# Optimization experiments

Hardware: AMD Instinct MI355X
Metric: run time of the kernel (lower is better)

## Reference

```python
import jax, jax.numpy as jnp
import numpy as np

N, IN, OUT, K = 4096, 512, 256, 3
ALPHA, BETA, ETA = 0.2, 0.1, 0.5
NEG_INF = -9e15


def setup_inputs() -> dict:
    key = jax.random.key(0)
    k1, k2, k3, k4, k5, k6 = jax.random.split(key, 6)
    h = jax.random.normal(k1, (N, IN), dtype=jnp.float32)
    # xavier-ish scale for params
    W = jax.random.normal(k2, (K * IN, OUT), dtype=jnp.float32) * (1.414 / np.sqrt(IN + OUT))
    a = jax.random.normal(k3, (2 * OUT * K, 1), dtype=jnp.float32) * 0.05
    disc = jax.random.normal(k4, (2 * OUT, 1), dtype=jnp.float32) * 0.05
    k_mask = jax.random.randint(k5, (K, N, N), 0, 2).astype(jnp.int32)  # 0/1 k-hop masks
    lamda = jax.random.uniform(k6, (1,), dtype=jnp.float32)
    return {"h": h, "W": W, "a": a, "disc": disc, "k_mask": k_mask, "lamda": lamda}


def reference(h, W, a, disc, k_mask, lamda):
    lam = lamda[0]
    Wk = W.reshape(K, IN, OUT)          # W[i*IN:(i+1)*IN] per hop
    ak = a.reshape(K, 2, OUT)           # a[2*hop*OUT:(2*hop+2)*OUT] per hop, split in two
    d = disc.reshape(2, OUT)

    # Per-hop projections. In the torch loop Wh is recomputed from h each hop,
    # so only hop 0 determines the returned features; all hops feed dischange.
    Wh_all = jnp.einsum('ni,kio->kno', h, Wk)  # [K, N, OUT]

    # dischange = sum_i eta^i * (Wh_i @ d1 + (Wh_i @ d2).T)  -- rank-1 separable
    wts = ETA ** jnp.arange(K, dtype=jnp.float32)            # [K]
    dv1 = jnp.einsum('kno,o->kn', Wh_all, d[0])              # [K, N]
    dv2 = jnp.einsum('kno,o->kn', Wh_all, d[1])
    u = jnp.einsum('k,kn->n', wts, dv1)
    v = jnp.einsum('k,kn->n', wts, dv2)
    dischange = u[:, None] + v[None, :]                      # [N, N]

    # hop-0 masked GAT attention
    Wh0 = Wh_all[0]
    s1 = Wh0 @ ak[0, 0]                                      # [N]
    s2 = Wh0 @ ak[0, 1]
    e = jax.nn.leaky_relu(s1[:, None] + s2[None, :], ALPHA)  # [N, N]
    att = jax.nn.softmax(jnp.where(k_mask[0] > 0, e, NEG_INF), axis=1)
    # dropout disabled (eval mode / training=False)
    Wh = (1.0 - BETA) * (att @ Wh0) + BETA * Wh0
    out = jax.nn.elu(Wh)

    # normalize dischange and threshold against lamda
    dn = dischange / jnp.maximum(jnp.abs(dischange.min()), dischange.max())
    pos = (dn > lam).astype(jnp.int32)
    dn = jnp.where(dn > lam, 0.0, dn)
    neg = (dn < -lam).astype(jnp.int32)
    dn = jnp.where(dn < -lam, 0.0, dn)

    # mask lists computed from ORIGINAL masks, then applied sequentially
    pos_list = [((k_mask[i] + pos) >= 2).astype(jnp.int32) for i in range(K - 1)]
    neg_list = [((k_mask[i] + neg) >= 2).astype(jnp.int32) for i in range(1, K)]
    km = k_mask
    for i in range(1, K):
        km = km.at[i].add(pos_list[i - 1])
        km = km.at[i - 1].add(-pos_list[i - 1])
    for i in range(K - 1):
        km = km.at[i + 1].add(neg_list[i])
        km = km.at[i].add(-neg_list[i])

    return out, dn, km
```

## Files before the change

### kernel.cpp

```cpp
#include <hip/hip_runtime.h>
#include <hip/hip_bf16.h>
#include <math.h>

#define N 4096
#define DIN 512
#define DOUT 256

typedef short bf16x8 __attribute__((ext_vector_type(8)));
typedef float f32x4 __attribute__((ext_vector_type(4)));

static __device__ __forceinline__ unsigned short f2bf(float x) {
  __hip_bfloat16 b = __float2bfloat16(x);
  return __builtin_bit_cast(unsigned short, b);
}

__global__ __launch_bounds__(256) void k_pq(const float* __restrict__ W,
                                            const float* __restrict__ disc,
                                            double* __restrict__ p, double* __restrict__ q) {
  __shared__ double lds[8];
  int i = blockIdx.x;
  int t = threadIdx.x;
  double accp = 0.0, accq = 0.0;
  const double wts[3] = {1.0, 0.5, 0.25};
#pragma unroll
  for (int k = 0; k < 3; ++k) {
    double w = (double)W[((size_t)(k * DIN + i)) * DOUT + t];
    accp += wts[k] * w * (double)disc[t];
    accq += wts[k] * w * (double)disc[DOUT + t];
  }
  for (int off = 32; off; off >>= 1) { accp += __shfl_down(accp, off); accq += __shfl_down(accq, off); }
  int l = t & 63, w_ = t >> 6;
  if (l == 0) { lds[w_] = accp; lds[4 + w_] = accq; }
  __syncthreads();
  if (t == 0) {
    p[i] = lds[0] + lds[1] + lds[2] + lds[3];
    q[i] = lds[4] + lds[5] + lds[6] + lds[7];
  }
}

__global__ __launch_bounds__(256) void k_uv(const float* __restrict__ h,
                                            const double* __restrict__ p, const double* __restrict__ q,
                                            double* __restrict__ u, double* __restrict__ v) {
  __shared__ double lds[8];
  int n = blockIdx.x, t = threadIdx.x;
  double su = 0.0, sv = 0.0;
#pragma unroll
  for (int i = t; i < DIN; i += 256) {
    double hv = (double)h[(size_t)n * DIN + i];
    su += hv * p[i];
    sv += hv * q[i];
  }
  for (int off = 32; off; off >>= 1) { su += __shfl_down(su, off); sv += __shfl_down(sv, off); }
  int l = t & 63, w_ = t >> 6;
  if (l == 0) { lds[w_] = su; lds[4 + w_] = sv; }
  __syncthreads();
  if (t == 0) {
    u[n] = lds[0] + lds[1] + lds[2] + lds[3];
    v[n] = lds[4] + lds[5] + lds[6] + lds[7];
  }
}

__global__ __launch_bounds__(1024) void k_denom(const double* __restrict__ u,
                                                const double* __restrict__ v,
                                                double* __restrict__ scal) {
  __shared__ double lds[64];
  int t = threadIdx.x;
  double mnu = 1e300, mxu = -1e300, mnv = 1e300, mxv = -1e300;
#pragma unroll
  for (int k = 0; k < 4; ++k) {
    double uu = u[t + k * 1024], vv = v[t + k * 1024];
    mnu = fmin(mnu, uu); mxu = fmax(mxu, uu);
    mnv = fmin(mnv, vv); mxv = fmax(mxv, vv);
  }
  for (int off = 32; off; off >>= 1) {
    mnu = fmin(mnu, __shfl_down(mnu, off)); mxu = fmax(mxu, __shfl_down(mxu, off));
    mnv = fmin(mnv, __shfl_down(mnv, off)); mxv = fmax(mxv, __shfl_down(mxv, off));
  }
  int l = t & 63, w_ = t >> 6;
  if (l == 0) { lds[w_] = mnu; lds[16 + w_] = mxu; lds[32 + w_] = mnv; lds[48 + w_] = mxv; }
  __syncthreads();
  if (t == 0) {
    double a = 1e300, b = -1e300, c = 1e300, d = -1e300;
    for (int k = 0; k < 16; ++k) {
      a = fmin(a, lds[k]); b = fmax(b, lds[16 + k]);
      c = fmin(c, lds[32 + k]); d = fmax(d, lds[48 + k]);
    }
    double mn = a + c, mx = b + d;
    double denom = fmax(fabs(mn), mx);
    scal[0] = 1.0 / denom;
  }
}

__global__ __launch_bounds__(256) void k_dnkm(const int* __restrict__ kmask,
                                              const double* __restrict__ u, const double* __restrict__ v,
                                              const double* __restrict__ scal, const float* __restrict__ lamda,
                                              float* __restrict__ dn, float* __restrict__ kmout) {
  const size_t NN = (size_t)N * N;
  const int* k0 = kmask; const int* k1 = kmask + NN; const int* k2 = kmask + 2 * NN;
  float* km0 = kmout; float* km1 = kmout + NN; float* km2 = kmout + 2 * NN;
  const size_t total4 = NN / 4;
  double inv = scal[0];
  double lam = (double)lamda[0];
  for (size_t idx = (size_t)blockIdx.x * 256 + threadIdx.x; idx < total4;
       idx += (size_t)gridDim.x * 256) {
    int i = (int)(idx >> 10);
    int j = (int)(idx & 1023) << 2;
    size_t base = (size_t)i * N + j;
    double ui = u[i];
    double2 va = *(const double2*)(v + j);
    double2 vb = *(const double2*)(v + j + 2);
    double vv[4] = {va.x, va.y, vb.x, vb.y};
    int4 m0 = *(const int4*)(k0 + base);
    int4 m1 = *(const int4*)(k1 + base);
    int4 m2 = *(const int4*)(k2 + base);
    float4 odn, o0, o1, o2;
#pragma unroll
    for (int c = 0; c < 4; ++c) {
      double dnv = (ui + vv[c]) * inv;
      bool pos = dnv > lam, neg = dnv < -lam;
      float dnf = (pos || neg) ? 0.0f : (float)dnv;
      int mk0 = (&m0.x)[c], mk1 = (&m1.x)[c], mk2 = (&m2.x)[c];
      int p0 = pos ? mk0 : 0;
      int p1 = pos ? mk1 : 0;
      int n0 = neg ? mk1 : 0;
      int n1 = neg ? mk2 : 0;
      (&odn.x)[c] = dnf;
      (&o0.x)[c] = (float)(mk0 - p0 - n0);
      (&o1.x)[c] = (float)(mk1 + p0 - p1 + n0 - n1);
      (&o2.x)[c] = (float)(mk2 + p1 + n1);
    }
    *(float4*)(dn + base) = odn;
    *(float4*)(km0 + base) = o0;
    *(float4*)(km1 + base) = o1;
    *(float4*)(km2 + base) = o2;
  }
}

__global__ __launch_bounds__(256) void k_wh0(const float* __restrict__ h, const float* __restrict__ W,
                                             float* __restrict__ Wh0, unsigned short* __restrict__ Wh0T) {
  __shared__ float As[64][20];
  __shared__ float Bs[16][72];
  int t = threadIdx.x;
  int i0 = blockIdx.x * 64, o0 = blockIdx.y * 64;
  int tx = t & 15, ty = t >> 4;
  float acc[4][4] = {};
  int am = t >> 2, ak = (t & 3) * 4;
  int bk = t >> 4, bn = (t & 15) * 4;
  for (int kb = 0; kb < DIN; kb += 16) {
    float4 av = *(const float4*)(h + (size_t)(i0 + am) * DIN + kb + ak);
    float4 bv = *(const float4*)(W + (size_t)(kb + bk) * DOUT + o0 + bn);
    *(float4*)&As[am][ak] = av;
    *(float4*)&Bs[bk][bn] = bv;
    __syncthreads();
#pragma unroll
    for (int kk = 0; kk < 16; ++kk) {
      float a0 = As[ty * 4 + 0][kk], a1 = As[ty * 4 + 1][kk];
      float a2 = As[ty * 4 + 2][kk], a3 = As[ty * 4 + 3][kk];
      float4 b = *(const float4*)&Bs[kk][tx * 4];
      acc[0][0] += a0 * b.x; acc[0][1] += a0 * b.y; acc[0][2] += a0 * b.z; acc[0][3] += a0 * b.w;
      acc[1][0] += a1 * b.x; acc[1][1] += a1 * b.y; acc[1][2] += a1 * b.z; acc[1][3] += a1 * b.w;
      acc[2][0] += a2 * b.x; acc[2][1] += a2 * b.y; acc[2][2] += a2 * b.z; acc[2][3] += a2 * b.w;
      acc[3][0] += a3 * b.x; acc[3][1] += a3 * b.y; acc[3][2] += a3 * b.z; acc[3][3] += a3 * b.w;
    }
    __syncthreads();
  }
#pragma unroll
  for (int r = 0; r < 4; ++r) {
    int n = i0 + ty * 4 + r;
    float4 vo = {acc[r][0], acc[r][1], acc[r][2], acc[r][3]};
    *(float4*)(Wh0 + (size_t)n * DOUT + o0 + tx * 4) = vo;
#pragma unroll
    for (int c = 0; c < 4; ++c) {
      Wh0T[(size_t)(o0 + tx * 4 + c) * N + n] = f2bf(acc[r][c]);
    }
  }
}

__global__ __launch_bounds__(256) void k_s1s2(const float* __restrict__ Wh0, const float* __restrict__ a,
                                              float* __restrict__ s1, float* __restrict__ s2) {
  __shared__ float lds[8];
  int i = blockIdx.x, t = threadIdx.x;
  float val = Wh0[(size_t)i * DOUT + t];
  float v1 = val * a[t];
  float v2 = val * a[DOUT + t];
  for (int off = 32; off; off >>= 1) { v1 += __shfl_down(v1, off); v2 += __shfl_down(v2, off); }
  int l = t & 63, w_ = t >> 6;
  if (l == 0) { lds[w_] = v1; lds[4 + w_] = v2; }
  __syncthreads();
  if (t == 0) {
    s1[i] = lds[0] + lds[1] + lds[2] + lds[3];
    s2[i] = lds[4] + lds[5] + lds[6] + lds[7];
  }
}

__global__ __launch_bounds__(256) void k_rowstats(const int* __restrict__ k0,
                                                  const float* __restrict__ s1, const float* __restrict__ s2,
                                                  float* __restrict__ mrow, float* __restrict__ zinv,
                                                  int* __restrict__ flag) {
  __shared__ float earr[N];
  __shared__ float redf[4];
  __shared__ int redi[4];
  __shared__ float bm; __shared__ int bc;
  int i = blockIdx.x, t = threadIdx.x;
  float s1i = s1[i];
  float lmax = -1e30f; int lcnt = 0;
  for (int j = t; j < N; j += 256) {
    int mk = k0[(size_t)i * N + j];
    float sv = s1i + s2[j];
    float e = sv >= 0.0f ? sv : 0.2f * sv;
    bool um = mk > 0;
    earr[j] = um ? e : -1e30f;
    if (um) { lmax = fmaxf(lmax, e); lcnt++; }
  }
  for (int off = 32; off; off >>= 1) { lmax = fmaxf(lmax, __shfl_down(lmax, off)); lcnt += __shfl_down(lcnt, off); }
  int l = t & 63, w_ = t >> 6;
  if (l == 0) { redf[w_] = lmax; redi[w_] = lcnt; }
  __syncthreads();
  if (t == 0) {
    bm = fmaxf(fmaxf(redf[0], redf[1]), fmaxf(redf[2], redf[3]));
    bc = redi[0] + redi[1] + redi[2] + redi[3];
  }
  __syncthreads();
  float m = bm; int c = bc;
  float lsum = 0.0f;
  if (c > 0) {
    for (int j = t; j < N; j += 256) {
      float e = earr[j];
      if (e > -1e29f) lsum += expf(e - m);
    }
  }
  for (int off = 32; off; off >>= 1) lsum += __shfl_down(lsum, off);
  if (l == 0) redf[w_] = lsum;
  __syncthreads();
  if (t == 0) {
    float Z = redf[0] + redf[1] + redf[2] + redf[3];
    if (c == 0) { mrow[i] = 0.0f; zinv[i] = 1.0f / (float)N; flag[i] = 1; }
    else        { mrow[i] = m;    zinv[i] = 1.0f / Z;        flag[i] = 0; }
  }
}

__global__ __launch_bounds__(256) void k_attn(const int* __restrict__ k0,
                                              const float* __restrict__ s1, const float* __restrict__ s2,
                                              const float* __restrict__ mrow, const float* __restrict__ zinv,
                                              const int* __restrict__ flag,
                                              const float* __restrict__ Wh0, const unsigned short* __restrict__ Wh0T,
                                              float* __restrict__ out) {
  __shared__ unsigned short Ats[16][40];
  int t = threadIdx.x;
  int i0 = blockIdx.x * 16;
  int l = t & 63, w = t >> 6;
  int o0 = w * 64;
  int r = t & 15, c2 = t >> 4;
  int irow = i0 + r;
  float s1r = s1[irow], mr = mrow[irow];
  int fl = flag[irow];
  const int* mptr = k0 + (size_t)irow * N + c2 * 2;
  f32x4 acc[4] = {f32x4{0,0,0,0}, f32x4{0,0,0,0}, f32x4{0,0,0,0}, f32x4{0,0,0,0}};
  const unsigned short* bbase = Wh0T + ((size_t)(o0 + (l & 15)) * N + 8 * (l >> 4));
  bf16x8 bn0 = *(const bf16x8*)(bbase + 0 * 16 * N);
  bf16x8 bn1 = *(const bf16x8*)(bbase + 1 * 16 * N);
  bf16x8 bn2 = *(const bf16x8*)(bbase + 2 * 16 * N);
  bf16x8 bn3 = *(const bf16x8*)(bbase + 3 * 16 * N);
  for (int j0 = 0; j0 < N; j0 += 32) {
    int2 mk = *(const int2*)(mptr + j0);
    int j = j0 + c2 * 2;
    float e0 = s1r + s2[j];     e0 = e0 >= 0.0f ? e0 : 0.2f * e0;
    float e1 = s1r + s2[j + 1]; e1 = e1 >= 0.0f ? e1 : 0.2f * e1;
    float p0 = fl ? 1.0f : (mk.x > 0 ? expf(e0 - mr) : 0.0f);
    float p1 = fl ? 1.0f : (mk.y > 0 ? expf(e1 - mr) : 0.0f);
    unsigned int packed = (unsigned int)f2bf(p0) | ((unsigned int)f2bf(p1) << 16);
    *(unsigned int*)(&Ats[r][c2 * 2]) = packed;
    bf16x8 bc0 = bn0, bc1 = bn1, bc2 = bn2, bc3 = bn3;
    if (j0 + 32 < N) {
      const unsigned short* nb = bbase + (j0 + 32);
      bn0 = *(const bf16x8*)(nb + 0 * 16 * N);
      bn1 = *(const bf16x8*)(nb + 1 * 16 * N);
      bn2 = *(const bf16x8*)(nb + 2 * 16 * N);
      bn3 = *(const bf16x8*)(nb + 3 * 16 * N);
    }
    __syncthreads();
    bf16x8 af = *(const bf16x8*)(&Ats[l & 15][8 * (l >> 4)]);
    acc[0] = __builtin_amdgcn_mfma_f32_16x16x32_bf16(af, bc0, acc[0], 0, 0, 0);
    acc[1] = __builtin_amdgcn_mfma_f32_16x16x32_bf16(af, bc1, acc[1], 0, 0, 0);
    acc[2] = __builtin_amdgcn_mfma_f32_16x16x32_bf16(af, bc2, acc[2], 0, 0, 0);
    acc[3] = __builtin_amdgcn_mfma_f32_16x16x32_bf16(af, bc3, acc[3], 0, 0, 0);
    __syncthreads();
  }
  int col = l & 15, rw = (l >> 4) * 4;
#pragma unroll
  for (int reg = 0; reg < 4; ++reg) {
    int i = i0 + rw + reg;
    float zi = zinv[i];
#pragma unroll
    for (int os = 0; os < 4; ++os) {
      int o = o0 + os * 16 + col;
      float accv = acc[os][reg];
      float val = 0.9f * accv * zi + 0.1f * Wh0[(size_t)i * DOUT + o];
      out[(size_t)i * DOUT + o] = val > 0.0f ? val : expm1f(val);
    }
  }
}

extern "C" void kernel_launch(void* const* d_in, const int* in_sizes, int n_in,
                              void* d_out, int out_size, void* d_ws, size_t ws_size,
                              hipStream_t stream) {
  const float* h     = (const float*)d_in[0];
  const float* W     = (const float*)d_in[1];
  const float* a     = (const float*)d_in[2];
  const float* disc  = (const float*)d_in[3];
  const int*   kmask = (const int*)d_in[4];
  const float* lamda = (const float*)d_in[5];

  float* out = (float*)d_out;
  float* dn  = out + (size_t)N * DOUT;
  float* km  = dn + (size_t)N * N;

  char* ws = (char*)d_ws;
  double* p    = (double*)ws;
  double* q    = (double*)(ws + 4096);
  double* u    = (double*)(ws + 8192);
  double* v    = (double*)(ws + 8192 + 32768);
  double* scal = (double*)(ws + 8192 + 65536);
  char* ws2 = ws + 8192 + 65536 + 256;
  float* s1   = (float*)ws2;
  float* s2   = (float*)(ws2 + 16384);
  float* mrow = (float*)(ws2 + 32768);
  float* zin  = (float*)(ws2 + 49152);
  int*   flag = (int*)(ws2 + 65536);
  float* Wh0  = (float*)(ws2 + 65536 + 16384);
  unsigned short* Wh0T = (unsigned short*)(ws2 + 65536 + 16384 + (size_t)N * DOUT * 4);

  k_pq<<<DIN, 256, 0, stream>>>(W, disc, p, q);
  k_uv<<<N, 256, 0, stream>>>(h, p, q, u, v);
  k_denom<<<1, 1024, 0, stream>>>(u, v, scal);
  k_dnkm<<<4096, 256, 0, stream>>>(kmask, u, v, scal, lamda, dn, km);
  k_wh0<<<dim3(64, 4), 256, 0, stream>>>(h, W, Wh0, Wh0T);
  k_s1s2<<<N, 256, 0, stream>>>(Wh0, a, s1, s2);
  k_rowstats<<<N, 256, 0, stream>>>(kmask, s1, s2, mrow, zin, flag);
  k_attn<<<N / 16, 256, 0, stream>>>(kmask, s1, s2, mrow, zin, flag, Wh0, Wh0T, out);
}
```

Before: 616.6 us.

## Split attention GEMM over key dimension and drop LDS staging in A-fragment build

The attention-times-Wh0 kernel now splits the key dimension into eight chunks across a second grid axis. Each block writes a partial accumulator, and a new reduction kernel sums the partials and applies the normalisation, residual and ELU. Each lane now builds its own MFMA A fragment straight from vectorised mask and s2 loads, which removes the shared-memory staging and both barriers per iteration. The goal is more blocks than the original 256 to fill the GPU, at the cost of an extra N×256×8 float workspace round-trip, another launch, and dropping the software prefetch of B.

```diff
diff --git a/kernel.cpp b/kernel.cpp
--- a/kernel.cpp
+++ b/kernel.cpp
@@ -5,6 +5,8 @@
 #define N 4096
 #define DIN 512
 #define DOUT 256
+#define JS 8
+#define JCH (N / JS)
 
 typedef short bf16x8 __attribute__((ext_vector_type(8)));
 typedef float f32x4 __attribute__((ext_vector_type(4)));
@@ -239,66 +241,79 @@
   }
 }
 
-__global__ __launch_bounds__(256) void k_attn(const int* __restrict__ k0,
-                                              const float* __restrict__ s1, const float* __restrict__ s2,
-                                              const float* __restrict__ mrow, const float* __restrict__ zinv,
-                                              const int* __restrict__ flag,
-                                              const float* __restrict__ Wh0, const unsigned short* __restrict__ Wh0T,
-                                              float* __restrict__ out) {
-  __shared__ unsigned short Ats[16][40];
+__global__ __launch_bounds__(256) void k_attn2(const int* __restrict__ k0,
+                                               const float* __restrict__ s1, const float* __restrict__ s2,
+                                               const float* __restrict__ mrow, const int* __restrict__ flag,
+                                               const unsigned short* __restrict__ Wh0T,
+                                               float* __restrict__ Opart) {
   int t = threadIdx.x;
   int i0 = blockIdx.x * 16;
-  int l = t & 63, w = t >> 6;
+  int w = t >> 6, l = t & 63;
   int o0 = w * 64;
-  int r = t & 15, c2 = t >> 4;
-  int irow = i0 + r;
+  int row = l & 15;
+  int kg = l >> 4;
+  int irow = i0 + row;
   float s1r = s1[irow], mr = mrow[irow];
   int fl = flag[irow];
-  const int* mptr = k0 + (size_t)irow * N + c2 * 2;
-  f32x4 acc[4] = {f32x4{0,0,0,0}, f32x4{0,0,0,0}, f32x4{0,0,0,0}, f32x4{0,0,0,0}};
-  const unsigned short* bbase = Wh0T + ((size_t)(o0 + (l & 15)) * N + 8 * (l >> 4));
-  bf16x8 bn0 = *(const bf16x8*)(bbase + 0 * 16 * N);
-  bf16x8 bn1 = *(const bf16x8*)(bbase + 1 * 16 * N);
-  bf16x8 bn2 = *(const bf16x8*)(bbase + 2 * 16 * N);
-  bf16x8 bn3 = *(const bf16x8*)(bbase + 3 * 16 * N);
-  for (int j0 = 0; j0 < N; j0 += 32) {
-    int2 mk = *(const int2*)(mptr + j0);
-    int j = j0 + c2 * 2;
-    float e0 = s1r + s2[j];     e0 = e0 >= 0.0f ? e0 : 0.2f * e0;
-    float e1 = s1r + s2[j + 1]; e1 = e1 >= 0.0f ? e1 : 0.2f * e1;
-    float p0 = fl ? 1.0f : (mk.x > 0 ? expf(e0 - mr) : 0.0f);
-    float p1 = fl ? 1.0f : (mk.y > 0 ? expf(e1 - mr) : 0.0f);
-    unsigned int packed = (unsigned int)f2bf(p0) | ((unsigned int)f2bf(p1) << 16);
-    *(unsigned int*)(&Ats[r][c2 * 2]) = packed;
-    bf16x8 bc0 = bn0, bc1 = bn1, bc2 = bn2, bc3 = bn3;
-    if (j0 + 32 < N) {
-      const unsigned short* nb = bbase + (j0 + 32);
-      bn0 = *(const bf16x8*)(nb + 0 * 16 * N);
-      bn1 = *(const bf16x8*)(nb + 1 * 16 * N);
-      bn2 = *(const bf16x8*)(nb + 2 * 16 * N);
-      bn3 = *(const bf16x8*)(nb + 3 * 16 * N);
-    }
-    __syncthreads();
-    bf16x8 af = *(const bf16x8*)(&Ats[l & 15][8 * (l >> 4)]);
-    acc[0] = __builtin_amdgcn_mfma_f32_16x16x32_bf16(af, bc0, acc[0], 0, 0, 0);
-    acc[1] = __builtin_amdgcn_mfma_f32_16x16x32_bf16(af, bc1, acc[1], 0, 0, 0);
-    acc[2] = __builtin_amdgcn_mfma_f32_16x16x32_bf16(af, bc2, acc[2], 0, 0, 0);
-    acc[3] = __builtin_amdgcn_mfma_f32_16x16x32_bf16(af, bc3, acc[3], 0, 0, 0);
-    __syncthreads();
-  }
+  f32x4 acc0 = {0,0,0,0}, acc1 = {0,0,0,0}, acc2 = {0,0,0,0}, acc3 = {0,0,0,0};
+  const unsigned short* bbase = Wh0T + ((size_t)(o0 + row) * N + 8 * kg);
+  const int* mbase = k0 + (size_t)irow * N + 8 * kg;
+  const float* sbase = s2 + 8 * kg;
+  int jbeg = blockIdx.y * JCH;
+  for (int j0 = jbeg; j0 < jbeg + JCH; j0 += 32) {
+    int4 ma = *(const int4*)(mbase + j0);
+    int4 mb = *(const int4*)(mbase + j0 + 4);
+    float4 sa = *(const float4*)(sbase + j0);
+    float4 sb = *(const float4*)(sbase + j0 + 4);
+    float pv[8];
+#pragma unroll
+    for (int c = 0; c < 4; ++c) {
+      float sv = s1r + (&sa.x)[c];
+      float e = sv >= 0.0f ? sv : 0.2f * sv;
+      pv[c] = fl ? 1.0f : ((&ma.x)[c] > 0 ? expf(e - mr) : 0.0f);
+    }
+#pragma unroll
+    for (int c = 0; c < 4; ++c) {
+      float sv = s1r + (&sb.x)[c];
+      float e = sv >= 0.0f ? sv : 0.2f * sv;
+      pv[4 + c] = fl ? 1.0f : ((&mb.x)[c] > 0 ? expf(e - mr) : 0.0f);
+    }
+    bf16x8 af;
+#pragma unroll
+    for (int c = 0; c < 8; ++c) af[c] = (short)f2bf(pv[c]);
+    bf16x8 b0 = *(const bf16x8*)(bbase + j0);
+    bf16x8 b1 = *(const bf16x8*)(bbase + 16 * N + j0);
+    bf16x8 b2 = *(const bf16x8*)(bbase + 32 * N + j0);
+    bf16x8 b3 = *(const bf16x8*)(bbase + 48 * N + j0);
+    acc0 = __builtin_amdgcn_mfma_f32_16x16x32_bf16(af, b0, acc0, 0, 0, 0);
+    acc1 = __builtin_amdgcn_mfma_f32_16x16x32_bf16(af, b1, acc1, 0, 0, 0);
+    acc2 = __builtin_amdgcn_mfma_f32_16x16x32_bf16(af, b2, acc2, 0, 0, 0);
+    acc3 = __builtin_amdgcn_mfma_f32_16x16x32_bf16(af, b3, acc3, 0, 0, 0);
+  }
+  float* op = Opart + (size_t)blockIdx.y * N * DOUT;
   int col = l & 15, rw = (l >> 4) * 4;
+  f32x4 accs[4] = {acc0, acc1, acc2, acc3};
 #pragma unroll
   for (int reg = 0; reg < 4; ++reg) {
     int i = i0 + rw + reg;
-    float zi = zinv[i];
 #pragma unroll
     for (int os = 0; os < 4; ++os) {
-      int o = o0 + os * 16 + col;
-      float accv = acc[os][reg];
-      float val = 0.9f * accv * zi + 0.1f * Wh0[(size_t)i * DOUT + o];
-      out[(size_t)i * DOUT + o] = val > 0.0f ? val : expm1f(val);
-    }
-  }
+      op[(size_t)i * DOUT + o0 + os * 16 + col] = accs[os][reg];
+    }
+  }
+}
+
+__global__ __launch_bounds__(256) void k_ored(const float* __restrict__ Opart,
+                                              const float* __restrict__ Wh0,
+                                              const float* __restrict__ zinv,
+                                              float* __restrict__ out) {
+  int i = blockIdx.x, t = threadIdx.x;
+  size_t idx = (size_t)i * DOUT + t;
+  float s = 0.0f;
+#pragma unroll
+  for (int by = 0; by < JS; ++by) s += Opart[(size_t)by * N * DOUT + idx];
+  float val = 0.9f * s * zinv[i] + 0.1f * Wh0[idx];
+  out[idx] = val > 0.0f ? val : expm1f(val);
 }
 
 extern "C" void kernel_launch(void* const* d_in, const int* in_sizes, int n_in,
@@ -329,6 +344,7 @@
   int*   flag = (int*)(ws2 + 65536);
   float* Wh0  = (float*)(ws2 + 65536 + 16384);
   unsigned short* Wh0T = (unsigned short*)(ws2 + 65536 + 16384 + (size_t)N * DOUT * 4);
+  float* Opart = (float*)(ws2 + 65536 + 16384 + (size_t)N * DOUT * 4 + (size_t)N * DOUT * 2);
 
   k_pq<<<DIN, 256, 0, stream>>>(W, disc, p, q);
   k_uv<<<N, 256, 0, stream>>>(h, p, q, u, v);
@@ -337,5 +353,6 @@
   k_wh0<<<dim3(64, 4), 256, 0, stream>>>(h, W, Wh0, Wh0T);
   k_s1s2<<<N, 256, 0, stream>>>(Wh0, a, s1, s2);
   k_rowstats<<<N, 256, 0, stream>>>(kmask, s1, s2, mrow, zin, flag);
-  k_attn<<<N / 16, 256, 0, stream>>>(kmask, s1, s2, mrow, zin, flag, Wh0, Wh0T, out);
-}
+  k_attn2<<<dim3(N / 16, JS), 256, 0, stream>>>(kmask, s1, s2, mrow, flag, Wh0T, Opart);
+  k_ored<<<N, 256, 0, stream>>>(Opart, Wh0, zin, out);
+}
```

Result: no change. 621.4 us (+0.8%).
